# Kernel tuning notes

Measured on AMD Instinct MI355X. Metric: run time of the kernel, lower is better.

## Reference

```python
import jax, jax.numpy as jnp
import numpy as np
import math

V, E, H, L, S_MAX = 50257, 1024, 16, 4, 1024
D = E // H
F = 4 * E
B, S = 2, 1024


def _ln(x, w, b, eps=1e-5):
    mu = jnp.mean(x, axis=-1, keepdims=True)
    var = jnp.var(x, axis=-1, keepdims=True)
    return (x - mu) * jax.lax.rsqrt(var + eps) * w + b


def setup_inputs() -> dict:
    key = jax.random.key(0)
    ks = jax.random.split(key, 16)
    std = 0.02
    def nrm(k, shape):
        return jax.random.normal(k, shape, dtype=jnp.float32) * std
    inp = {
        'idx': jax.random.randint(ks[0], (B, S), 0, V),
        'tok_emb': nrm(ks[1], (V, E)),
        'pos_emb': jnp.zeros((S_MAX, E), jnp.float32),
        # per-layer stacked params; Linear weights stored [in, out]
        'ln1_w': jnp.ones((L, E), jnp.float32), 'ln1_b': jnp.zeros((L, E), jnp.float32),
        'Wq': nrm(ks[2], (L, E, E)), 'bq': jnp.zeros((L, E), jnp.float32),
        'Wk': nrm(ks[3], (L, E, E)), 'bk': jnp.zeros((L, E), jnp.float32),
        'Wv': nrm(ks[4], (L, E, E)), 'bv': jnp.zeros((L, E), jnp.float32),
        'Wo': nrm(ks[5], (L, E, E)), 'bo': jnp.zeros((L, E), jnp.float32),
        'ln2_w': jnp.ones((L, E), jnp.float32), 'ln2_b': jnp.zeros((L, E), jnp.float32),
        'W1': nrm(ks[6], (L, E, F)), 'b1': jnp.zeros((L, F), jnp.float32),
        'W2': nrm(ks[7], (L, F, E)), 'b2': jnp.zeros((L, E), jnp.float32),
        'lnf_w': jnp.ones((E,), jnp.float32), 'lnf_b': jnp.zeros((E,), jnp.float32),
        'head_W': nrm(ks[8], (V, E)),  # torch Linear weight [out, in], no bias
    }
    return inp


def _gpt(idx, tok_emb, pos_emb, ln1_w, ln1_b, Wq, bq, Wk, bk, Wv, bv, Wo, bo,
         ln2_w, ln2_b, W1, b1, W2, b2, lnf_w, lnf_b, head_W):
    b, s = idx.shape
    x = tok_emb[idx] + pos_emb[None, :s, :]  # [B,S,E]
    causal = jnp.tril(jnp.ones((s, s), bool))
    scale = 1.0 / math.sqrt(D)
    for l in range(L):
        h = _ln(x, ln1_w[l], ln1_b[l])
        q = (h @ Wq[l] + bq[l]).reshape(b, s, H, D).transpose(0, 2, 1, 3)
        k = (h @ Wk[l] + bk[l]).reshape(b, s, H, D).transpose(0, 2, 1, 3)
        v = (h @ Wv[l] + bv[l]).reshape(b, s, H, D).transpose(0, 2, 1, 3)
        scores = jnp.einsum('bhsd,bhtd->bhst', q, k) * scale
        scores = jnp.where(causal, scores, -jnp.inf)
        attn = jax.nn.softmax(scores, axis=-1)
        y = jnp.einsum('bhst,bhtd->bhsd', attn, v)
        y = y.transpose(0, 2, 1, 3).reshape(b, s, E)
        x = x + y @ Wo[l] + bo[l]
        h2 = _ln(x, ln2_w[l], ln2_b[l])
        x = x + jax.nn.gelu(h2 @ W1[l] + b1[l], approximate=False) @ W2[l] + b2[l]
    x = _ln(x, lnf_w, lnf_b)
    return x @ head_W.T  # logits [B,S,V]


def reference(idx, tok_emb, pos_emb, ln1_w, ln1_b, Wq, bq, Wk, bk, Wv, bv, Wo, bo,
              ln2_w, ln2_b, W1, b1, W2, b2, lnf_w, lnf_b, head_W):
    return _gpt(idx, tok_emb, pos_emb, ln1_w, ln1_b, Wq, bq, Wk, bk, Wv, bv, Wo, bo,
                ln2_w, ln2_b, W1, b1, W2, b2, lnf_w, lnf_b, head_W)
```

## Files before the change

### kernel.cpp

```cpp
#include <hip/hip_runtime.h>
#include <hip/hip_bf16.h>
#include <math.h>

#define E_DIM 1024
#define H_NUM 16
#define D_DIM 64
#define F_DIM 4096
#define L_NUM 4
#define B_NUM 2
#define S_LEN 1024
#define V_DIM 50257
#define M_TOK 2048

typedef __attribute__((ext_vector_type(8))) short s8v;
typedef __attribute__((ext_vector_type(4))) float f4v;

static __device__ __forceinline__ float bf2f(unsigned short u) {
    union { unsigned int i; float f; } c; c.i = ((unsigned int)u) << 16; return c.f;
}
static __device__ __forceinline__ unsigned short f2bf(float f) {
    union { float f; unsigned int i; } c; c.f = f;
    unsigned int r = c.i + 0x7FFFu + ((c.i >> 16) & 1u);
    return (unsigned short)(r >> 16);
}

static __device__ __forceinline__ void gload16(const ushort* g, ushort* l) {
    __builtin_amdgcn_global_load_lds(
        (const __attribute__((address_space(1))) unsigned int*)g,
        (__attribute__((address_space(3))) unsigned int*)l, 16, 0, 0);
}

__global__ void embed_kernel(const int* __restrict__ idx,
                             const float* __restrict__ tok,
                             const float* __restrict__ pos,
                             float* __restrict__ x) {
    int row = blockIdx.x;
    int s = row & (S_LEN - 1);
    int t = idx[row];
    const float* te = tok + (size_t)t * E_DIM;
    const float* pe = pos + (size_t)s * E_DIM;
    float* xr = x + (size_t)row * E_DIM;
    int c = threadIdx.x * 4;
    float4 a = *(const float4*)(te + c);
    float4 p = *(const float4*)(pe + c);
    float4 o; o.x = a.x + p.x; o.y = a.y + p.y; o.z = a.z + p.z; o.w = a.w + p.w;
    *(float4*)(xr + c) = o;
}

__global__ void ln_kernel(const float* __restrict__ x,
                          const float* __restrict__ w,
                          const float* __restrict__ b,
                          ushort* __restrict__ out) {
    int row = blockIdx.x;
    const float* xr = x + (size_t)row * E_DIM;
    int tid = threadIdx.x;
    float4 v = *(const float4*)(xr + tid * 4);
    float s  = v.x + v.y + v.z + v.w;
    float s2 = v.x*v.x + v.y*v.y + v.z*v.z + v.w*v.w;
    #pragma unroll
    for (int m = 32; m >= 1; m >>= 1) {
        s  += __shfl_xor(s,  m, 64);
        s2 += __shfl_xor(s2, m, 64);
    }
    __shared__ float red[8];
    int wid = tid >> 6;
    if ((tid & 63) == 0) { red[wid] = s; red[wid + 4] = s2; }
    __syncthreads();
    s  = red[0] + red[1] + red[2] + red[3];
    s2 = red[4] + red[5] + red[6] + red[7];
    float mu  = s * (1.0f / E_DIM);
    float var = s2 * (1.0f / E_DIM) - mu * mu;
    float rs  = rsqrtf(var + 1e-5f);
    float4 wv = *(const float4*)(w + tid * 4);
    float4 bv = *(const float4*)(b + tid * 4);
    ushort4 o;
    o.x = f2bf((v.x - mu) * rs * wv.x + bv.x);
    o.y = f2bf((v.y - mu) * rs * wv.y + bv.y);
    o.z = f2bf((v.z - mu) * rs * wv.z + bv.z);
    o.w = f2bf((v.w - mu) * rs * wv.w + bv.w);
    *(ushort4*)(out + (size_t)row * E_DIM + tid * 4) = o;
}

static __device__ __forceinline__ void tconv_body(
    const float* __restrict__ in, ushort* __restrict__ out, int K, int N, int bx, int by)
{
    __shared__ ushort t[64][72];
    int n0 = bx * 64, k0 = by * 64;
    int tid = threadIdx.x;
    int r = tid >> 4, c = (tid & 15) * 4;
    #pragma unroll
    for (int it = 0; it < 4; ++it) {
        int kl = it * 16 + r;
        float4 v = *(const float4*)(in + (size_t)(k0 + kl) * N + n0 + c);
        t[kl][c]   = f2bf(v.x); t[kl][c+1] = f2bf(v.y);
        t[kl][c+2] = f2bf(v.z); t[kl][c+3] = f2bf(v.w);
    }
    __syncthreads();
    int nl = tid >> 2, k8 = (tid & 3) * 16;
    s8v o0, o1;
    #pragma unroll
    for (int j = 0; j < 8; ++j) o0[j] = (short)t[k8 + j][nl];
    #pragma unroll
    for (int j = 0; j < 8; ++j) o1[j] = (short)t[k8 + 8 + j][nl];
    *(s8v*)(out + (size_t)(n0 + nl) * K + k0 + k8)     = o0;
    *(s8v*)(out + (size_t)(n0 + nl) * K + k0 + k8 + 8) = o1;
}

__global__ __launch_bounds__(256) void tconv_kernel(const float* __restrict__ in,
                                                    ushort* __restrict__ out, int K, int N) {
    tconv_body(in, out, K, N, blockIdx.x, blockIdx.y);
}

__global__ __launch_bounds__(256) void tconv_qkvo_all(
    const float* __restrict__ Wq, const float* __restrict__ Wk,
    const float* __restrict__ Wv, const float* __restrict__ Wo,
    ushort* __restrict__ out)
{
    int z = blockIdx.z, l = z >> 2, w = z & 3;
    const float* in = (w == 0 ? Wq : w == 1 ? Wk : w == 2 ? Wv : Wo)
                      + (size_t)l * E_DIM * E_DIM;
    tconv_body(in, out + (size_t)z * E_DIM * E_DIM, E_DIM, E_DIM, blockIdx.x, blockIdx.y);
}

__global__ __launch_bounds__(256) void tconv_w_all(
    const float* __restrict__ W, ushort* __restrict__ out, int K, int N)
{
    int l = blockIdx.z;
    tconv_body(W + (size_t)l * K * N, out + (size_t)l * K * N, K, N, blockIdx.x, blockIdx.y);
}

__global__ void conv_kernel(const float* __restrict__ in, ushort* __restrict__ out, int n) {
    int i = (blockIdx.x * 256 + threadIdx.x) * 8;
    if (i + 8 <= n) {
        float4 a = *(const float4*)(in + i);
        float4 b = *(const float4*)(in + i + 4);
        s8v o;
        o[0]=(short)f2bf(a.x); o[1]=(short)f2bf(a.y); o[2]=(short)f2bf(a.z); o[3]=(short)f2bf(a.w);
        o[4]=(short)f2bf(b.x); o[5]=(short)f2bf(b.y); o[6]=(short)f2bf(b.z); o[7]=(short)f2bf(b.w);
        *(s8v*)(out + i) = o;
    }
}

#define KSTR 72
__global__ __launch_bounds__(256) void attn_mfma_kernel(
    const ushort* __restrict__ qg, const ushort* __restrict__ kg,
    const ushort* __restrict__ vg, ushort* __restrict__ yg)
{
    __shared__ ushort Ks[64][KSTR];
    __shared__ ushort Vt[64][KSTR];
    __shared__ ushort Ps[4][16][KSTR];

    int tid = threadIdx.x;
    int wid = tid >> 6, lane = tid & 63;
    int c = lane & 15, g = lane >> 4;

    int head = blockIdx.x & 31;
    int qt = 15 - (blockIdx.x >> 5);
    int b = head >> 4, h = head & 15;
    int qw = qt * 64 + wid * 16;
    size_t base = (size_t)b * S_LEN * E_DIM + (size_t)(h * D_DIM);

    s8v qf[2];
    #pragma unroll
    for (int ks = 0; ks < 2; ++ks)
        qf[ks] = *(const s8v*)(qg + base + (size_t)(qw + c) * E_DIM + ks * 32 + g * 8);

    f4v o[4];
    #pragma unroll
    for (int dt = 0; dt < 4; ++dt) o[dt] = (f4v){0.f, 0.f, 0.f, 0.f};
    float m[4], lsum[4];
    #pragma unroll
    for (int j = 0; j < 4; ++j) { m[j] = -1e30f; lsum[j] = 0.f; }

    for (int tt = 0; tt <= qt; ++tt) {
        int t0 = tt * 64;
        #pragma unroll
        for (int it = 0; it < 2; ++it) {
            int ch = tid + it * 256;
            int tr = ch >> 3, dc = (ch & 7) << 3;
            s8v kv = *(const s8v*)(kg + base + (size_t)(t0 + tr) * E_DIM + dc);
            *(s8v*)(&Ks[tr][dc]) = kv;
            s8v vv = *(const s8v*)(vg + base + (size_t)(t0 + tr) * E_DIM + dc);
            int tsw = tr ^ ((ch & 7) << 3);
            #pragma unroll
            for (int j = 0; j < 8; ++j)
                Vt[dc + j][tsw] = (ushort)vv[j];
        }
        __syncthreads();

        f4v s4[4];
        #pragma unroll
        for (int tj = 0; tj < 4; ++tj) {
            s4[tj] = (f4v){0.f, 0.f, 0.f, 0.f};
            #pragma unroll
            for (int ks = 0; ks < 2; ++ks) {
                s8v kf = *(const s8v*)(&Ks[tj * 16 + c][ks * 32 + g * 8]);
                s4[tj] = __builtin_amdgcn_mfma_f32_16x16x32_bf16(qf[ks], kf, s4[tj], 0, 0, 0);
            }
        }

        bool diag = (tt == qt);
        float sc[4][4], pm[4];
        #pragma unroll
        for (int j = 0; j < 4; ++j) pm[j] = -1e30f;
        #pragma unroll
        for (int tj = 0; tj < 4; ++tj)
            #pragma unroll
            for (int j = 0; j < 4; ++j) {
                float val = s4[tj][j] * 0.125f;
                if (diag) {
                    int t_loc = tj * 16 + c;
                    int q_loc = wid * 16 + 4 * g + j;
                    if (t_loc > q_loc) val = -1e30f;
                }
                sc[tj][j] = val;
                pm[j] = fmaxf(pm[j], val);
            }
        #pragma unroll
        for (int msk = 1; msk <= 8; msk <<= 1)
            #pragma unroll
            for (int j = 0; j < 4; ++j)
                pm[j] = fmaxf(pm[j], __shfl_xor(pm[j], msk, 64));
        float rs[4], corr[4];
        #pragma unroll
        for (int j = 0; j < 4; ++j) {
            float nm = fmaxf(m[j], pm[j]);
            corr[j] = __expf(m[j] - nm);
            m[j] = nm;
            rs[j] = 0.f;
        }
        #pragma unroll
        for (int tj = 0; tj < 4; ++tj)
            #pragma unroll
            for (int j = 0; j < 4; ++j) {
                float p = __expf(sc[tj][j] - m[j]);
                rs[j] += p;
                Ps[wid][4 * g + j][(tj * 16 + c) ^ (g << 3)] = f2bf(p);
            }
        #pragma unroll
        for (int msk = 1; msk <= 8; msk <<= 1)
            #pragma unroll
            for (int j = 0; j < 4; ++j)
                rs[j] += __shfl_xor(rs[j], msk, 64);
        #pragma unroll
        for (int j = 0; j < 4; ++j) lsum[j] = lsum[j] * corr[j] + rs[j];
        #pragma unroll
        for (int dt = 0; dt < 4; ++dt)
            #pragma unroll
            for (int j = 0; j < 4; ++j) o[dt][j] *= corr[j];

        #pragma unroll
        for (int ks = 0; ks < 2; ++ks) {
            int blk = g + 4 * ks;
            int pblk = blk ^ (c >> 2);
            s8v pa = *(const s8v*)(&Ps[wid][c][pblk << 3]);
            #pragma unroll
            for (int dt = 0; dt < 4; ++dt) {
                int d = dt * 16 + c;
                int vblk = blk ^ ((d >> 3) & 7);
                s8v vb = *(const s8v*)(&Vt[d][vblk << 3]);
                o[dt] = __builtin_amdgcn_mfma_f32_16x16x32_bf16(pa, vb, o[dt], 0, 0, 0);
            }
        }
        __syncthreads();
    }

    float inv[4];
    #pragma unroll
    for (int j = 0; j < 4; ++j) inv[j] = 1.f / lsum[j];
    #pragma unroll
    for (int dt = 0; dt < 4; ++dt)
        #pragma unroll
        for (int j = 0; j < 4; ++j)
            yg[base + (size_t)(qw + 4 * g + j) * E_DIM + dt * 16 + c] = f2bf(o[dt][j] * inv[j]);
}

template<int EPI>
static __device__ __forceinline__ void gemm_bb_body(
    const ushort* __restrict__ A, const ushort* __restrict__ B,
    const float* __restrict__ bias, const float* __restrict__ res,
    float* __restrict__ outF, ushort* __restrict__ outB,
    int Ndim, int Kdim, int m0, int n0, int nRows)
{
    __shared__ ushort As[128 * 64];
    __shared__ ushort Bs[128 * 64];
    int tid = threadIdx.x;
    int wid = tid >> 6, lane = tid & 63;
    int wr = wid >> 1, wc = wid & 1;
    int fr = lane & 15, fq = lane >> 4;
    int lr = lane >> 3, ls = lane & 7;

    f4v acc[4][4];
    #pragma unroll
    for (int mi = 0; mi < 4; ++mi)
        #pragma unroll
        for (int ni = 0; ni < 4; ++ni)
            acc[mi][ni] = (f4v){0.f, 0.f, 0.f, 0.f};

    for (int k0 = 0; k0 < Kdim; k0 += 64) {
        #pragma unroll
        for (int it = 0; it < 4; ++it) {
            int r = wid * 32 + it * 8 + lr;
            int ss = ls ^ (r & 7);
            gload16(A + (size_t)(m0 + r) * Kdim + k0 + ss * 8,
                    As + r * 64 - lr * 64 - ls * 8);
        }
        #pragma unroll
        for (int it = 0; it < 4; ++it) {
            int r = wid * 32 + it * 8 + lr;
            int ss = ls ^ (r & 7);
            int br = n0 + r; if (br >= nRows) br = nRows - 1;
            gload16(B + (size_t)br * Kdim + k0 + ss * 8,
                    Bs + r * 64 - lr * 64 - ls * 8);
        }
        __syncthreads();
        #pragma unroll
        for (int ks = 0; ks < 2; ++ks) {
            s8v af[4], bfv[4];
            #pragma unroll
            for (int mi = 0; mi < 4; ++mi) {
                int Ra = wr * 64 + mi * 16 + fr;
                int Sa = (ks * 4 + fq) ^ (fr & 7);
                af[mi] = *(const s8v*)(As + Ra * 64 + Sa * 8);
            }
            #pragma unroll
            for (int ni = 0; ni < 4; ++ni) {
                int Rb = wc * 64 + ni * 16 + fr;
                int Sb = (ks * 4 + fq) ^ (fr & 7);
                bfv[ni] = *(const s8v*)(Bs + Rb * 64 + Sb * 8);
            }
            #pragma unroll
            for (int mi = 0; mi < 4; ++mi)
                #pragma unroll
                for (int ni = 0; ni < 4; ++ni)
                    acc[mi][ni] = __builtin_amdgcn_mfma_f32_16x16x32_bf16(
                        af[mi], bfv[ni], acc[mi][ni], 0, 0, 0);
        }
        __syncthreads();
    }

    #pragma unroll
    for (int mi = 0; mi < 4; ++mi) {
        int row = m0 + wr * 64 + mi * 16 + fq * 4;
        #pragma unroll
        for (int ni = 0; ni < 4; ++ni) {
            int col = n0 + wc * 64 + ni * 16 + fr;
            float bv = 0.f;
            if (EPI == 0 || EPI == 1 || EPI == 2) bv = bias[col];
            #pragma unroll
            for (int j = 0; j < 4; ++j) {
                float val = acc[mi][ni][j] + bv;
                size_t off = (size_t)(row + j) * Ndim + col;
                if (EPI == 0) {
                    outB[off] = f2bf(val);
                } else if (EPI == 1) {
                    outF[off] = res[off] + val;
                } else if (EPI == 2) {
                    val = 0.5f * val * (1.f + erff(val * 0.70710678118654752f));
                    outB[off] = f2bf(val);
                } else {
                    if (col < Ndim) outF[off] = val;
                }
            }
        }
    }
}

template<int EPI>
__global__ __launch_bounds__(256) void gemm_bb_kernel(
    const ushort* __restrict__ A, const ushort* __restrict__ B,
    const float* __restrict__ bias, const float* __restrict__ res,
    float* __restrict__ outF, ushort* __restrict__ outB,
    int Ndim, int Kdim, int nRows)
{
    int x = blockIdx.x & 7, i = blockIdx.x >> 3;
    int mb = x * 2 + (i & 1), nb = i >> 1;
    gemm_bb_body<EPI>(A, B, bias, res, outF, outB, Ndim, Kdim, mb * 128, nb * 128, nRows);
}

__global__ __launch_bounds__(256) void gemm_qkv_bb_kernel(
    const ushort* __restrict__ A,
    const ushort* __restrict__ Bq, const ushort* __restrict__ Bk, const ushort* __restrict__ Bv,
    const float* __restrict__ bq, const float* __restrict__ bk, const float* __restrict__ bv,
    ushort* __restrict__ oq, ushort* __restrict__ ok, ushort* __restrict__ ov)
{
    int x = blockIdx.x & 7, i = blockIdx.x >> 3;
    int sel = i >> 4, j = i & 15;
    int mb = x * 2 + (j & 1), nb = j >> 1;
    const ushort* B   = (sel == 0) ? Bq : (sel == 1) ? Bk : Bv;
    const float* bias = (sel == 0) ? bq : (sel == 1) ? bk : bv;
    ushort* o         = (sel == 0) ? oq : (sel == 1) ? ok : ov;
    gemm_bb_body<0>(A, B, bias, nullptr, nullptr, o, E_DIM, E_DIM, mb * 128, nb * 128, E_DIM);
}

template<int EPI>
static __device__ __forceinline__ void gemm64_body(
    const ushort* __restrict__ A, const ushort* __restrict__ B,
    const float* __restrict__ bias, const float* __restrict__ res,
    float* __restrict__ outF, ushort* __restrict__ outB,
    int Ndim, int Kdim, int m0, int n0)
{
    __shared__ ushort As[64 * 64];
    __shared__ ushort Bs[128 * 64];
    int tid = threadIdx.x;
    int wid = tid >> 6, lane = tid & 63;
    int fr = lane & 15, fq = lane >> 4;
    int lr = lane >> 3, ls = lane & 7;

    f4v acc[4][2];
    #pragma unroll
    for (int mi = 0; mi < 4; ++mi)
        #pragma unroll
        for (int ni = 0; ni < 2; ++ni)
            acc[mi][ni] = (f4v){0.f, 0.f, 0.f, 0.f};

    for (int k0 = 0; k0 < Kdim; k0 += 64) {
        #pragma unroll
        for (int it = 0; it < 2; ++it) {
            int r = wid * 16 + it * 8 + lr;
            int ss = ls ^ (r & 7);
            gload16(A + (size_t)(m0 + r) * Kdim + k0 + ss * 8,
                    As + r * 64 - lr * 64 - ls * 8);
        }
        #pragma unroll
        for (int it = 0; it < 4; ++it) {
            int r = wid * 32 + it * 8 + lr;
            int ss = ls ^ (r & 7);
            gload16(B + (size_t)(n0 + r) * Kdim + k0 + ss * 8,
                    Bs + r * 64 - lr * 64 - ls * 8);
        }
        __syncthreads();
        #pragma unroll
        for (int ks = 0; ks < 2; ++ks) {
            s8v af[4], bfv[2];
            #pragma unroll
            for (int mi = 0; mi < 4; ++mi) {
                int Ra = mi * 16 + fr;
                int Sa = (ks * 4 + fq) ^ (fr & 7);
                af[mi] = *(const s8v*)(As + Ra * 64 + Sa * 8);
            }
            #pragma unroll
            for (int ni = 0; ni < 2; ++ni) {
                int Rb = wid * 32 + ni * 16 + fr;
                int Sb = (ks * 4 + fq) ^ (fr & 7);
                bfv[ni] = *(const s8v*)(Bs + Rb * 64 + Sb * 8);
            }
            #pragma unroll
            for (int mi = 0; mi < 4; ++mi)
                #pragma unroll
                for (int ni = 0; ni < 2; ++ni)
                    acc[mi][ni] = __builtin_amdgcn_mfma_f32_16x16x32_bf16(
                        af[mi], bfv[ni], acc[mi][ni], 0, 0, 0);
        }
        __syncthreads();
    }

    #pragma unroll
    for (int mi = 0; mi < 4; ++mi) {
        int row = m0 + mi * 16 + fq * 4;
        #pragma unroll
        for (int ni = 0; ni < 2; ++ni) {
            int col = n0 + wid * 32 + ni * 16 + fr;
            float bv = bias[col];
            #pragma unroll
            for (int j = 0; j < 4; ++j) {
                float val = acc[mi][ni][j] + bv;
                size_t off = (size_t)(row + j) * Ndim + col;
                if (EPI == 0) {
                    outB[off] = f2bf(val);
                } else {
                    outF[off] = res[off] + val;
                }
            }
        }
    }
}

template<int EPI>
__global__ __launch_bounds__(256) void gemm64_kernel(
    const ushort* __restrict__ A, const ushort* __restrict__ B,
    const float* __restrict__ bias, const float* __restrict__ res,
    float* __restrict__ outF, ushort* __restrict__ outB,
    int Ndim, int Kdim)
{
    int x = blockIdx.x & 7, i = blockIdx.x >> 3;
    int mb = x * 4 + (i & 3), nb = i >> 2;
    gemm64_body<EPI>(A, B, bias, res, outF, outB, Ndim, Kdim, mb * 64, nb * 128);
}

__global__ __launch_bounds__(256) void gemm64_qkv_kernel(
    const ushort* __restrict__ A, const ushort* __restrict__ Wall,
    const float* __restrict__ bq, const float* __restrict__ bk, const float* __restrict__ bv,
    ushort* __restrict__ oq, ushort* __restrict__ ok, ushort* __restrict__ ov)
{
    int x = blockIdx.x & 7, i = blockIdx.x >> 3;
    int sel = i >> 5, j = i & 31;
    int mb = x * 4 + (j & 3), nb = j >> 2;
    const ushort* B   = Wall + (size_t)sel * E_DIM * E_DIM;
    const float* bias = (sel == 0) ? bq : (sel == 1) ? bk : bv;
    ushort* o         = (sel == 0) ? oq : (sel == 1) ? ok : ov;
    gemm64_body<0>(A, B, bias, nullptr, nullptr, o, E_DIM, E_DIM, mb * 64, nb * 128);
}

extern "C" void kernel_launch(void* const* d_in, const int* in_sizes, int n_in,
                              void* d_out, int out_size, void* d_ws, size_t ws_size,
                              hipStream_t stream) {
    (void)in_sizes; (void)n_in; (void)out_size;
    const int*   idx  = (const int*)d_in[0];
    const float* tok  = (const float*)d_in[1];
    const float* pos  = (const float*)d_in[2];
    const float* ln1w = (const float*)d_in[3];
    const float* ln1b = (const float*)d_in[4];
    const float* Wq   = (const float*)d_in[5];
    const float* bq   = (const float*)d_in[6];
    const float* Wk   = (const float*)d_in[7];
    const float* bk   = (const float*)d_in[8];
    const float* Wv   = (const float*)d_in[9];
    const float* bv   = (const float*)d_in[10];
    const float* Wo   = (const float*)d_in[11];
    const float* bo   = (const float*)d_in[12];
    const float* ln2w = (const float*)d_in[13];
    const float* ln2b = (const float*)d_in[14];
    const float* W1   = (const float*)d_in[15];
    const float* b1   = (const float*)d_in[16];
    const float* W2   = (const float*)d_in[17];
    const float* b2   = (const float*)d_in[18];
    const float* lnfw = (const float*)d_in[19];
    const float* lnfb = (const float*)d_in[20];
    const float* headW= (const float*)d_in[21];
    float* out = (float*)d_out;

    char* ws = (char*)d_ws;
    float*  x  = (float*)(ws);
    ushort* h  = (ushort*)(ws + 8u  * 1024 * 1024);
    ushort* qb = (ushort*)(ws + 12u * 1024 * 1024);
    ushort* kb = (ushort*)(ws + 16u * 1024 * 1024);
    ushort* vb = (ushort*)(ws + 20u * 1024 * 1024);
    ushort* yb = (ushort*)(ws + 24u * 1024 * 1024);
    ushort* ub = (ushort*)(ws + 28u * 1024 * 1024);
    ushort* wqb = (ushort*)(ws + 44u * 1024 * 1024);
    ushort* wkb = (ushort*)(ws + 46u * 1024 * 1024);
    ushort* wvb = (ushort*)(ws + 48u * 1024 * 1024);
    ushort* wob = (ushort*)(ws + 50u * 1024 * 1024);
    ushort* w1b = (ushort*)(ws + 52u * 1024 * 1024);
    ushort* w2b = (ushort*)(ws + 60u * 1024 * 1024);
    ushort* hdbM = (ushort*)(ws + 68u * 1024 * 1024);
    ushort* wall  = (ushort*)(ws + 44u  * 1024 * 1024);
    ushort* w1all = (ushort*)(ws + 76u  * 1024 * 1024);
    ushort* w2all = (ushort*)(ws + 108u * 1024 * 1024);
    ushort* hdbH  = (ushort*)(ws + 140u * 1024 * 1024);

    size_t headB = (size_t)V_DIM * E_DIM * 2;
    bool huge = ws_size >= 140ull * 1024 * 1024 + headB;
    bool big  = ws_size >= 68ull * 1024 * 1024 + headB;
    bool mid  = ws_size >= 68ull * 1024 * 1024;

    dim3 blk(256);
    embed_kernel<<<dim3(M_TOK), blk, 0, stream>>>(idx, tok, pos, x);

    if (huge) {
        tconv_qkvo_all<<<dim3(16, 16, 16), blk, 0, stream>>>(Wq, Wk, Wv, Wo, wall);
        tconv_w_all<<<dim3(64, 16, 4), blk, 0, stream>>>(W1, w1all, E_DIM, F_DIM);
        tconv_w_all<<<dim3(16, 64, 4), blk, 0, stream>>>(W2, w2all, F_DIM, E_DIM);
        int n = V_DIM * E_DIM;
        conv_kernel<<<dim3((n / 8 + 255) / 256), blk, 0, stream>>>(headW, hdbH, n);

        for (int l = 0; l < L_NUM; ++l) {
            const ushort* wl  = wall  + (size_t)(l * 4) * E_DIM * E_DIM;
            const ushort* wol = wall  + (size_t)(l * 4 + 3) * E_DIM * E_DIM;
            const ushort* w1l = w1all + (size_t)l * E_DIM * F_DIM;
            const ushort* w2l = w2all + (size_t)l * F_DIM * E_DIM;

            ln_kernel<<<dim3(M_TOK), blk, 0, stream>>>(x, ln1w + l * E_DIM, ln1b + l * E_DIM, h);
            gemm64_qkv_kernel<<<dim3(768), blk, 0, stream>>>(h, wl,
                bq + l*E_DIM, bk + l*E_DIM, bv + l*E_DIM, qb, kb, vb);
            attn_mfma_kernel<<<dim3(512), blk, 0, stream>>>(qb, kb, vb, yb);
            gemm64_kernel<1><<<dim3(256), blk, 0, stream>>>(yb, wol, bo + l*E_DIM, x, x, nullptr, E_DIM, E_DIM);
            ln_kernel<<<dim3(M_TOK), blk, 0, stream>>>(x, ln2w + l * E_DIM, ln2b + l * E_DIM, h);
            gemm_bb_kernel<2><<<dim3(512), blk, 0, stream>>>(h, w1l, b1 + l*F_DIM, nullptr, nullptr, ub, F_DIM, E_DIM, F_DIM);
            gemm64_kernel<1><<<dim3(256), blk, 0, stream>>>(ub, w2l, b2 + l*E_DIM, x, x, nullptr, E_DIM, F_DIM);
        }
        ln_kernel<<<dim3(M_TOK), blk, 0, stream>>>(x, lnfw, lnfb, h);
        gemm_bb_kernel<3><<<dim3(6288), blk, 0, stream>>>(h, hdbH, nullptr, nullptr, out, nullptr, V_DIM, E_DIM, V_DIM);
        return;
    }

    if (big) {
        int n = V_DIM * E_DIM;
        conv_kernel<<<dim3((n / 8 + 255) / 256), blk, 0, stream>>>(headW, hdbM, n);
    }

    for (int l = 0; l < L_NUM; ++l) {
        const float* wq = Wq + (size_t)l * E_DIM * E_DIM;
        const float* wk = Wk + (size_t)l * E_DIM * E_DIM;
        const float* wv = Wv + (size_t)l * E_DIM * E_DIM;
        const float* wo = Wo + (size_t)l * E_DIM * E_DIM;
        const float* w1 = W1 + (size_t)l * E_DIM * F_DIM;
        const float* w2 = W2 + (size_t)l * F_DIM * E_DIM;

        ln_kernel<<<dim3(M_TOK), blk, 0, stream>>>(x, ln1w + l * E_DIM, ln1b + l * E_DIM, h);
        if (mid) {
            tconv_kernel<<<dim3(16, 16), blk, 0, stream>>>(wq, wqb, E_DIM, E_DIM);
            tconv_kernel<<<dim3(16, 16), blk, 0, stream>>>(wk, wkb, E_DIM, E_DIM);
            tconv_kernel<<<dim3(16, 16), blk, 0, stream>>>(wv, wvb, E_DIM, E_DIM);
            tconv_kernel<<<dim3(16, 16), blk, 0, stream>>>(wo, wob, E_DIM, E_DIM);
            tconv_kernel<<<dim3(64, 16), blk, 0, stream>>>(w1, w1b, E_DIM, F_DIM);
            tconv_kernel<<<dim3(16, 64), blk, 0, stream>>>(w2, w2b, F_DIM, E_DIM);

            gemm_qkv_bb_kernel<<<dim3(384), blk, 0, stream>>>(h, wqb, wkb, wvb,
                bq + l*E_DIM, bk + l*E_DIM, bv + l*E_DIM, qb, kb, vb);
            attn_mfma_kernel<<<dim3(512), blk, 0, stream>>>(qb, kb, vb, yb);
            gemm_bb_kernel<1><<<dim3(128), blk, 0, stream>>>(yb, wob, bo + l*E_DIM, x, x, nullptr, E_DIM, E_DIM, E_DIM);
            ln_kernel<<<dim3(M_TOK), blk, 0, stream>>>(x, ln2w + l * E_DIM, ln2b + l * E_DIM, h);
            gemm_bb_kernel<2><<<dim3(512), blk, 0, stream>>>(h, w1b, b1 + l*F_DIM, nullptr, nullptr, ub, F_DIM, E_DIM, F_DIM);
            gemm_bb_kernel<1><<<dim3(128), blk, 0, stream>>>(ub, w2b, b2 + l*E_DIM, x, x, nullptr, E_DIM, F_DIM, E_DIM);
        }
    }

    ln_kernel<<<dim3(M_TOK), blk, 0, stream>>>(x, lnfw, lnfb, h);
    if (big) {
        gemm_bb_kernel<3><<<dim3(6288), blk, 0, stream>>>(h, hdbM, nullptr, nullptr, out, nullptr, V_DIM, E_DIM, V_DIM);
    }
}
```

Before: 1.231 ms.

## Split attention KV range across two wave groups with merged softmax state

```diff
diff --git a/kernel.cpp b/kernel.cpp
--- a/kernel.cpp
+++ b/kernel.cpp
@@ -142,22 +142,26 @@
 }
 
 #define KSTR 72
-__global__ __launch_bounds__(256) void attn_mfma_kernel(
+#define VSTR 144
+__global__ __launch_bounds__(512, 4) void attn_mfma_kernel(
     const ushort* __restrict__ qg, const ushort* __restrict__ kg,
     const ushort* __restrict__ vg, ushort* __restrict__ yg)
 {
-    __shared__ ushort Ks[64][KSTR];
-    __shared__ ushort Vt[64][KSTR];
-    __shared__ ushort Ps[4][16][KSTR];
+    __shared__ ushort smem[27648];
+    ushort (*Ks)[KSTR] = (ushort(*)[KSTR])smem;
+    ushort (*Vt)[VSTR] = (ushort(*)[VSTR])(smem + 128 * KSTR);
+    ushort (*Ps)[16][KSTR] = (ushort(*)[16][KSTR])(smem + 128 * KSTR + 64 * VSTR);
+    float* mb = (float*)smem;
 
     int tid = threadIdx.x;
     int wid = tid >> 6, lane = tid & 63;
     int c = lane & 15, g = lane >> 4;
+    int grp = wid >> 2, ws = wid & 3;
 
     int head = blockIdx.x & 31;
     int qt = 15 - (blockIdx.x >> 5);
     int b = head >> 4, h = head & 15;
-    int qw = qt * 64 + wid * 16;
+    int qw = qt * 64 + ws * 16;
     size_t base = (size_t)b * S_LEN * E_DIM + (size_t)(h * D_DIM);
 
     s8v qf[2];
@@ -172,107 +176,137 @@
     #pragma unroll
     for (int j = 0; j < 4; ++j) { m[j] = -1e30f; lsum[j] = 0.f; }
 
-    for (int tt = 0; tt <= qt; ++tt) {
-        int t0 = tt * 64;
+    int nr = (qt >> 1) + 1;
+    for (int r = 0; r < nr; ++r) {
+        int t0 = r * 128;
         #pragma unroll
         for (int it = 0; it < 2; ++it) {
-            int ch = tid + it * 256;
+            int ch = tid + it * 512;
             int tr = ch >> 3, dc = (ch & 7) << 3;
             s8v kv = *(const s8v*)(kg + base + (size_t)(t0 + tr) * E_DIM + dc);
             *(s8v*)(&Ks[tr][dc]) = kv;
             s8v vv = *(const s8v*)(vg + base + (size_t)(t0 + tr) * E_DIM + dc);
-            int tsw = tr ^ ((ch & 7) << 3);
+            int tsw = tr ^ dc;
             #pragma unroll
             for (int j = 0; j < 8; ++j)
                 Vt[dc + j][tsw] = (ushort)vv[j];
         }
         __syncthreads();
 
-        f4v s4[4];
-        #pragma unroll
-        for (int tj = 0; tj < 4; ++tj) {
-            s4[tj] = (f4v){0.f, 0.f, 0.f, 0.f};
+        int myt = r * 2 + grp;
+        if (myt <= qt) {
+            int toff = grp * 64;
+            f4v s4[4];
+            #pragma unroll
+            for (int tj = 0; tj < 4; ++tj) {
+                s4[tj] = (f4v){0.f, 0.f, 0.f, 0.f};
+                #pragma unroll
+                for (int ks = 0; ks < 2; ++ks) {
+                    s8v kf = *(const s8v*)(&Ks[toff + tj * 16 + c][ks * 32 + g * 8]);
+                    s4[tj] = __builtin_amdgcn_mfma_f32_16x16x32_bf16(qf[ks], kf, s4[tj], 0, 0, 0);
+                }
+            }
+
+            bool diag = (myt == qt);
+            float sc[4][4], pm[4];
+            #pragma unroll
+            for (int j = 0; j < 4; ++j) pm[j] = -1e30f;
+            #pragma unroll
+            for (int tj = 0; tj < 4; ++tj)
+                #pragma unroll
+                for (int j = 0; j < 4; ++j) {
+                    float val = s4[tj][j] * 0.125f;
+                    if (diag) {
+                        int t_loc = tj * 16 + c;
+                        int q_loc = ws * 16 + 4 * g + j;
+                        if (t_loc > q_loc) val = -1e30f;
+                    }
+                    sc[tj][j] = val;
+                    pm[j] = fmaxf(pm[j], val);
+                }
+            #pragma unroll
+            for (int msk = 1; msk <= 8; msk <<= 1)
+                #pragma unroll
+                for (int j = 0; j < 4; ++j)
+                    pm[j] = fmaxf(pm[j], __shfl_xor(pm[j], msk, 64));
+            float rs[4], corr[4];
+            #pragma unroll
+            for (int j = 0; j < 4; ++j) {
+                float nm = fmaxf(m[j], pm[j]);
+                corr[j] = __expf(m[j] - nm);
+                m[j] = nm;
+                rs[j] = 0.f;
+            }
+            #pragma unroll
+            for (int tj = 0; tj < 4; ++tj)
+                #pragma unroll
+                for (int j = 0; j < 4; ++j) {
+                    float p = __expf(sc[tj][j] - m[j]);
+                    rs[j] += p;
+                    Ps[wid][4 * g + j][(tj * 16 + c) ^ (g << 3)] = f2bf(p);
+                }
+            #pragma unroll
+            for (int msk = 1; msk <= 8; msk <<= 1)
+                #pragma unroll
+                for (int j = 0; j < 4; ++j)
+                    rs[j] += __shfl_xor(rs[j], msk, 64);
+            #pragma unroll
+            for (int j = 0; j < 4; ++j) lsum[j] = lsum[j] * corr[j] + rs[j];
+            #pragma unroll
+            for (int dt = 0; dt < 4; ++dt)
+                #pragma unroll
+                for (int j = 0; j < 4; ++j) o[dt][j] *= corr[j];
+
             #pragma unroll
             for (int ks = 0; ks < 2; ++ks) {
-                s8v kf = *(const s8v*)(&Ks[tj * 16 + c][ks * 32 + g * 8]);
-                s4[tj] = __builtin_amdgcn_mfma_f32_16x16x32_bf16(qf[ks], kf, s4[tj], 0, 0, 0);
-            }
-        }
-
-        bool diag = (tt == qt);
-        float sc[4][4], pm[4];
-        #pragma unroll
-        for (int j = 0; j < 4; ++j) pm[j] = -1e30f;
-        #pragma unroll
-        for (int tj = 0; tj < 4; ++tj)
+                int blk = g + 4 * ks;
+                int pblk = blk ^ (c >> 2);
+                s8v pa = *(const s8v*)(&Ps[wid][c][pblk << 3]);
+                int tb = grp * 8 + blk;
+                #pragma unroll
+                for (int dt = 0; dt < 4; ++dt) {
+                    int d = dt * 16 + c;
+                    int vblk = tb ^ ((d >> 3) & 7);
+                    s8v vb = *(const s8v*)(&Vt[d][vblk << 3]);
+                    o[dt] = __builtin_amdgcn_mfma_f32_16x16x32_bf16(pa, vb, o[dt], 0, 0, 0);
+                }
+            }
+        }
+        __syncthreads();
+    }
+
+    if (grp == 1) {
+        float* dst = mb + (ws * 64 + lane) * 25;
+        #pragma unroll
+        for (int j = 0; j < 4; ++j) { dst[j] = m[j]; dst[4 + j] = lsum[j]; }
+        #pragma unroll
+        for (int dt = 0; dt < 4; ++dt)
+            #pragma unroll
+            for (int j = 0; j < 4; ++j) dst[8 + dt * 4 + j] = o[dt][j];
+    }
+    __syncthreads();
+    if (grp == 0) {
+        const float* src = mb + (ws * 64 + lane) * 25;
+        float sA[4], sB[4];
+        #pragma unroll
+        for (int j = 0; j < 4; ++j) {
+            float mB = src[j], lB = src[4 + j];
+            float mN = fmaxf(m[j], mB);
+            sA[j] = __expf(m[j] - mN);
+            sB[j] = __expf(mB - mN);
+            lsum[j] = lsum[j] * sA[j] + lB * sB[j];
+        }
+        float inv[4];
+        #pragma unroll
+        for (int j = 0; j < 4; ++j) inv[j] = 1.f / lsum[j];
+        #pragma unroll
+        for (int dt = 0; dt < 4; ++dt)
             #pragma unroll
             for (int j = 0; j < 4; ++j) {
-                float val = s4[tj][j] * 0.125f;
-                if (diag) {
-                    int t_loc = tj * 16 + c;
-                    int q_loc = wid * 16 + 4 * g + j;
-                    if (t_loc > q_loc) val = -1e30f;
-                }
-                sc[tj][j] = val;
-                pm[j] = fmaxf(pm[j], val);
-            }
-        #pragma unroll
-        for (int msk = 1; msk <= 8; msk <<= 1)
-            #pragma unroll
-            for (int j = 0; j < 4; ++j)
-                pm[j] = fmaxf(pm[j], __shfl_xor(pm[j], msk, 64));
-        float rs[4], corr[4];
-        #pragma unroll
-        for (int j = 0; j < 4; ++j) {
-            float nm = fmaxf(m[j], pm[j]);
-            corr[j] = __expf(m[j] - nm);
-            m[j] = nm;
-            rs[j] = 0.f;
-        }
-        #pragma unroll
-        for (int tj = 0; tj < 4; ++tj)
-            #pragma unroll
-            for (int j = 0; j < 4; ++j) {
-                float p = __expf(sc[tj][j] - m[j]);
-                rs[j] += p;
-                Ps[wid][4 * g + j][(tj * 16 + c) ^ (g << 3)] = f2bf(p);
-            }
-        #pragma unroll
-        for (int msk = 1; msk <= 8; msk <<= 1)
-            #pragma unroll
-            for (int j = 0; j < 4; ++j)
-                rs[j] += __shfl_xor(rs[j], msk, 64);
-        #pragma unroll
-        for (int j = 0; j < 4; ++j) lsum[j] = lsum[j] * corr[j] + rs[j];
-        #pragma unroll
-        for (int dt = 0; dt < 4; ++dt)
-            #pragma unroll
-            for (int j = 0; j < 4; ++j) o[dt][j] *= corr[j];
-
-        #pragma unroll
-        for (int ks = 0; ks < 2; ++ks) {
-            int blk = g + 4 * ks;
-            int pblk = blk ^ (c >> 2);
-            s8v pa = *(const s8v*)(&Ps[wid][c][pblk << 3]);
-            #pragma unroll
-            for (int dt = 0; dt < 4; ++dt) {
-                int d = dt * 16 + c;
-                int vblk = blk ^ ((d >> 3) & 7);
-                s8v vb = *(const s8v*)(&Vt[d][vblk << 3]);
-                o[dt] = __builtin_amdgcn_mfma_f32_16x16x32_bf16(pa, vb, o[dt], 0, 0, 0);
-            }
-        }
-        __syncthreads();
-    }
-
-    float inv[4];
-    #pragma unroll
-    for (int j = 0; j < 4; ++j) inv[j] = 1.f / lsum[j];
-    #pragma unroll
-    for (int dt = 0; dt < 4; ++dt)
-        #pragma unroll
-        for (int j = 0; j < 4; ++j)
-            yg[base + (size_t)(qw + 4 * g + j) * E_DIM + dt * 16 + c] = f2bf(o[dt][j] * inv[j]);
+                float ov = o[dt][j] * sA[j] + src[8 + dt * 4 + j] * sB[j];
+                yg[base + (size_t)(qw + 4 * g + j) * E_DIM + dt * 16 + c] = f2bf(ov * inv[j]);
+            }
+    }
 }
 
 template<int EPI>
@@ -556,6 +590,7 @@
     bool mid  = ws_size >= 68ull * 1024 * 1024;
 
     dim3 blk(256);
+    dim3 blkA(512);
     embed_kernel<<<dim3(M_TOK), blk, 0, stream>>>(idx, tok, pos, x);
 
     if (huge) {
@@ -574,7 +609,7 @@
             ln_kernel<<<dim3(M_TOK), blk, 0, stream>>>(x, ln1w + l * E_DIM, ln1b + l * E_DIM, h);
             gemm64_qkv_kernel<<<dim3(768), blk, 0, stream>>>(h, wl,
                 bq + l*E_DIM, bk + l*E_DIM, bv + l*E_DIM, qb, kb, vb);
-            attn_mfma_kernel<<<dim3(512), blk, 0, stream>>>(qb, kb, vb, yb);
+            attn_mfma_kernel<<<dim3(512), blkA, 0, stream>>>(qb, kb, vb, yb);
             gemm64_kernel<1><<<dim3(256), blk, 0, stream>>>(yb, wol, bo + l*E_DIM, x, x, nullptr, E_DIM, E_DIM);
             ln_kernel<<<dim3(M_TOK), blk, 0, stream>>>(x, ln2w + l * E_DIM, ln2b + l * E_DIM, h);
             gemm_bb_kernel<2><<<dim3(512), blk, 0, stream>>>(h, w1l, b1 + l*F_DIM, nullptr, nullptr, ub, F_DIM, E_DIM, F_DIM);
@@ -609,7 +644,7 @@
 
             gemm_qkv_bb_kernel<<<dim3(384), blk, 0, stream>>>(h, wqb, wkb, wvb,
                 bq + l*E_DIM, bk + l*E_DIM, bv + l*E_DIM, qb, kb, vb);
-            attn_mfma_kernel<<<dim3(512), blk, 0, stream>>>(qb, kb, vb, yb);
+            attn_mfma_kernel<<<dim3(512), blkA, 0, stream>>>(qb, kb, vb, yb);
             gemm_bb_kernel<1><<<dim3(128), blk, 0, stream>>>(yb, wob, bo + l*E_DIM, x, x, nullptr, E_DIM, E_DIM, E_DIM);
             ln_kernel<<<dim3(M_TOK), blk, 0, stream>>>(x, ln2w + l * E_DIM, ln2b + l * E_DIM, h);
             gemm_bb_kernel<2><<<dim3(512), blk, 0, stream>>>(h, w1b, b1 + l*F_DIM, nullptr, nullptr, ub, F_DIM, E_DIM, F_DIM);
```

After: 1.173 ms. 1.05x faster.
